# Kernel tuning notes

Measured on AMD Instinct MI355X. Metric: run time of the kernel, lower is better.

The kernel has to match this reference:

```python
import jax, jax.numpy as jnp
import numpy as np
import math

B, S, H, NH = 2, 2048, 2048, 16
D = H // NH            # head dim = 128
FF = 4 * H
EPS = 1e-5


def layer_norm(x, w, b):
    mu = jnp.mean(x, axis=-1, keepdims=True)
    var = jnp.mean((x - mu) ** 2, axis=-1, keepdims=True)
    return (x - mu) * jax.lax.rsqrt(var + EPS) * w + b


def rotate_half(x):
    # split last dim into two halves (j=2 grouping), return (-x2, x1)
    x1, x2 = jnp.split(x, 2, axis=-1)
    return jnp.concatenate((-x2, x1), axis=-1)


def rope_freqs(seq_len, dim):
    inv_freq = 1.0 / (10000.0 ** (jnp.arange(0, dim, 2, dtype=jnp.float32) / dim))
    freqs = jnp.arange(seq_len, dtype=jnp.float32)[:, None] * inv_freq[None, :]
    return jnp.concatenate((freqs, freqs), axis=-1)  # [S, D]


def setup_inputs() -> dict:
    key = jax.random.key(0)
    ks = jax.random.split(key, 8)
    sc_h = 1.0 / math.sqrt(H)
    sc_ff = 1.0 / math.sqrt(FF)
    return {
        "hidden_states": jax.random.normal(ks[0], (B, S, H), jnp.float32),
        "attention_mask": jnp.zeros((1, 1, S, S), jnp.bool_),
        "ln1_w": jnp.ones((H,), jnp.float32),
        "ln1_b": jnp.zeros((H,), jnp.float32),
        "wqkv": jax.random.uniform(ks[1], (3 * H, H), jnp.float32, -sc_h, sc_h),
        "bqkv": jnp.zeros((3 * H,), jnp.float32),
        "wdense": jax.random.uniform(ks[2], (H, H), jnp.float32, -sc_h, sc_h),
        "bdense": jnp.zeros((H,), jnp.float32),
        "ln2_w": jnp.ones((H,), jnp.float32),
        "ln2_b": jnp.zeros((H,), jnp.float32),
        "w1": jax.random.uniform(ks[3], (FF, H), jnp.float32, -sc_h, sc_h),
        "b1": jnp.zeros((FF,), jnp.float32),
        "w2": jax.random.uniform(ks[4], (H, FF), jnp.float32, -sc_ff, sc_ff),
        "b2": jnp.zeros((H,), jnp.float32),
    }


def reference(hidden_states, attention_mask, ln1_w, ln1_b, wqkv, bqkv,
              wdense, bdense, ln2_w, ln2_b, w1, b1, w2, b2):
    residual = hidden_states
    x = layer_norm(hidden_states, ln1_w, ln1_b)

    qkv = jnp.einsum('bsh,oh->bso', x, wqkv) + bqkv           # [B,S,3H]
    qkv = qkv.reshape(B, S, NH, 3 * D).transpose(0, 2, 1, 3)  # [B,NH,S,3D]
    q, k, v = jnp.split(qkv, 3, axis=-1)                      # each [B,NH,S,D]

    pos = rope_freqs(S, D)                                    # [S,D]
    cos, sin = jnp.cos(pos), jnp.sin(pos)
    q = q * cos + rotate_half(q) * sin
    k = k * cos + rotate_half(k) * sin

    scale = 1.0 / math.sqrt(D)
    scores = jnp.einsum('bhqd,bhkd->bhqk', q, k) * scale      # [B,NH,S,S]
    causal = jnp.tril(jnp.ones((S, S), jnp.bool_))
    scores = jnp.where(causal, scores.astype(jnp.float32), -1e9)
    probs = jax.nn.softmax(scores, axis=-1).astype(v.dtype)

    ctx = jnp.einsum('bhqk,bhkd->bhqd', probs, v)             # [B,NH,S,D]
    ctx = ctx.transpose(0, 2, 1, 3).reshape(B, S, H)
    attn_out = jnp.einsum('bsh,oh->bso', ctx, wdense) + bdense

    hidden = residual + attn_out
    residual = hidden
    x = layer_norm(hidden, ln2_w, ln2_b)
    inter = jax.nn.gelu(jnp.einsum('bsh,fh->bsf', x, w1) + b1, approximate=False)
    out = jnp.einsum('bsf,hf->bsh', inter, w2) + b2
    hidden = residual + out
    return (hidden, attention_mask)
```

## Files before the change

### kernel.cpp

```cpp
#include <hip/hip_runtime.h>
#include <math.h>

typedef unsigned short u16;
typedef unsigned int u32;
typedef __attribute__((ext_vector_type(8))) __bf16 bf16x8;
typedef __attribute__((ext_vector_type(4))) float f32x4;
typedef __attribute__((ext_vector_type(8))) u16 u16x8;
typedef __attribute__((ext_vector_type(4))) u16 u16x4;

#define BB 2
#define SS 2048
#define HH 2048
#define NHH 16
#define DD 128
#define FFF 8192
#define MM (BB * SS)

__device__ __forceinline__ u16 f2bf(float f) {
  u32 u = __float_as_uint(f);
  u32 r = (u + 0x7FFFu + ((u >> 16) & 1u)) >> 16;
  return (u16)r;
}
__device__ __forceinline__ float b2f(u16 h) {
  return __uint_as_float(((u32)h) << 16);
}
__device__ __forceinline__ void gll16(const void* g, void* l) {
  __builtin_amdgcn_global_load_lds((const __attribute__((address_space(1))) void*)g,
                                   (__attribute__((address_space(3))) void*)l, 16, 0, 0);
}

struct CvtArgs {
  const float* src[4];
  u16* dst[4];
  int n[4];
};
__global__ __launch_bounds__(256) void cvt_all(CvtArgs a) {
  const int seg = blockIdx.y;
  const int i = (blockIdx.x * 256 + threadIdx.x) * 4;
  if (i + 3 < a.n[seg]) {
    f32x4 v = *(const f32x4*)(a.src[seg] + i);
    u16x4 o;
    o[0] = f2bf(v[0]); o[1] = f2bf(v[1]); o[2] = f2bf(v[2]); o[3] = f2bf(v[3]);
    *(u16x4*)(a.dst[seg] + i) = o;
  }
}

__global__ __launch_bounds__(256) void ln_bf16(const float* __restrict__ x,
                                               const float* __restrict__ w,
                                               const float* __restrict__ bsh,
                                               u16* __restrict__ out) {
  const int row = blockIdx.x, tid = threadIdx.x;
  const float* xr = x + (size_t)row * HH;
  f32x4 a = ((const f32x4*)xr)[tid * 2];
  f32x4 b = ((const f32x4*)xr)[tid * 2 + 1];
  float s = a[0] + a[1] + a[2] + a[3] + b[0] + b[1] + b[2] + b[3];
  float q = a[0]*a[0] + a[1]*a[1] + a[2]*a[2] + a[3]*a[3]
          + b[0]*b[0] + b[1]*b[1] + b[2]*b[2] + b[3]*b[3];
#pragma unroll
  for (int off = 32; off > 0; off >>= 1) {
    s += __shfl_down(s, off);
    q += __shfl_down(q, off);
  }
  __shared__ float red[8];
  const int wave = tid >> 6;
  if ((tid & 63) == 0) { red[wave] = s; red[4 + wave] = q; }
  __syncthreads();
  s = red[0] + red[1] + red[2] + red[3];
  q = red[4] + red[5] + red[6] + red[7];
  const float mean = s * (1.0f / HH);
  const float var = q * (1.0f / HH) - mean * mean;
  const float rstd = 1.0f / sqrtf(var + 1e-5f);
  f32x4 w0 = ((const f32x4*)w)[tid * 2];
  f32x4 w1 = ((const f32x4*)w)[tid * 2 + 1];
  f32x4 b0 = ((const f32x4*)bsh)[tid * 2];
  f32x4 b1 = ((const f32x4*)bsh)[tid * 2 + 1];
  u16x8 o;
#pragma unroll
  for (int i = 0; i < 4; ++i) o[i] = f2bf((a[i] - mean) * rstd * w0[i] + b0[i]);
#pragma unroll
  for (int i = 0; i < 4; ++i) o[4 + i] = f2bf((b[i] - mean) * rstd * w1[i] + b1[i]);
  *(u16x8*)(out + (size_t)row * HH + tid * 8) = o;
}

template <int MODE, int DB>
__global__ __launch_bounds__(256) void gemm_bt(const u16* __restrict__ A,
                                               const u16* __restrict__ Bw,
                                               const float* __restrict__ bias,
                                               const float* resid, void* Cout,
                                               int M, int N, int K) {
  __shared__ __align__(16) u16 As[DB ? 2 : 1][128 * 64];
  __shared__ __align__(16) u16 Bs[DB ? 2 : 1][128 * 64];
  const int tid = threadIdx.x;
  const int wave = tid >> 6, lane = tid & 63;
  const int l15 = lane & 15, quad = lane >> 4;
  const int bm = blockIdx.x, bn = blockIdx.y;
  const int wm = (wave >> 1) << 6, wn = (wave & 1) << 6;

  f32x4 acc[4][4] = {};

  const int srow = (wave << 5) + (lane >> 3);
  const int sg = (lane & 7) ^ (lane >> 3);
  const u16* aptr = A + (size_t)(bm * 128 + srow) * K + sg * 8;
  const u16* bptr = Bw + (size_t)(bn * 128 + srow) * K + sg * 8;

  auto stage = [&](int buf) {
#pragma unroll
    for (int i = 0; i < 4; ++i)
      gll16(aptr + (size_t)i * 8 * K, &As[buf][(wave * 4 + i) * 512]);
#pragma unroll
    for (int i = 0; i < 4; ++i)
      gll16(bptr + (size_t)i * 8 * K, &Bs[buf][(wave * 4 + i) * 512]);
    aptr += 64; bptr += 64;
  };

  auto compute = [&](int buf) {
#pragma unroll
    for (int tt = 0; tt < 2; ++tt) {
      bf16x8 af[4], bfv[4];
#pragma unroll
      for (int i = 0; i < 4; ++i) {
        const int m = wm + i * 16 + l15;
        const int n = wn + i * 16 + l15;
        const int gi = tt * 4 + quad;
        af[i] = *(const bf16x8*)&As[buf][m * 64 + ((gi ^ (m & 7)) << 3)];
        bfv[i] = *(const bf16x8*)&Bs[buf][n * 64 + ((gi ^ (n & 7)) << 3)];
      }
#pragma unroll
      for (int i = 0; i < 4; ++i)
#pragma unroll
        for (int j = 0; j < 4; ++j)
          acc[i][j] = __builtin_amdgcn_mfma_f32_16x16x32_bf16(af[i], bfv[j], acc[i][j], 0, 0, 0);
    }
  };

  const int nk = K >> 6;
  if constexpr (DB) {
    stage(0);
    for (int kt = 0; kt < nk; ++kt) {
      __syncthreads();
      if (kt + 1 < nk) stage((kt + 1) & 1);
      compute(kt & 1);
    }
  } else {
    for (int kt = 0; kt < nk; ++kt) {
      stage(0);
      __syncthreads();
      compute(0);
      __syncthreads();
    }
  }

#pragma unroll
  for (int i = 0; i < 4; ++i) {
    const int row0 = bm * 128 + wm + i * 16 + quad * 4;
#pragma unroll
    for (int j = 0; j < 4; ++j) {
      const int col = bn * 128 + wn + j * 16 + l15;
      const float bv = bias[col];
#pragma unroll
      for (int r = 0; r < 4; ++r) {
        const size_t idx = (size_t)(row0 + r) * N + col;
        float v = acc[i][j][r] + bv;
        if constexpr (MODE == 0) {
          ((u16*)Cout)[idx] = f2bf(v);
        } else if constexpr (MODE == 1) {
          ((float*)Cout)[idx] = v + resid[idx];
        } else {
          v = 0.5f * v * (1.0f + erff(v * 0.70710678118654752f));
          ((u16*)Cout)[idx] = f2bf(v);
        }
      }
    }
  }
}

#define PHASE256(QM, QN, STG, DW)                                                              \
  do {                                                                                         \
    bf16x8 af[4][2], bq[2][2];                                                                 \
    _Pragma("unroll") for (int im = 0; im < 4; ++im) {                                         \
      const int ar = wm * 128 + (QM) * 64 + im * 16 + l15;                                     \
      _Pragma("unroll") for (int tt = 0; tt < 2; ++tt)                                         \
          af[im][tt] = *(const bf16x8*)&as[ar * 64 + ((((tt << 2) + quad) ^ (ar & 7)) << 3)];  \
    }                                                                                          \
    _Pragma("unroll") for (int jn = 0; jn < 2; ++jn) {                                         \
      const int br = wn * 64 + (QN) * 32 + jn * 16 + l15;                                      \
      _Pragma("unroll") for (int tt = 0; tt < 2; ++tt)                                         \
          bq[jn][tt] = *(const bf16x8*)&bs[br * 64 + ((((tt << 2) + quad) ^ (br & 7)) << 3)];  \
    }                                                                                          \
    STG;                                                                                       \
    __builtin_amdgcn_s_barrier();                                                              \
    asm volatile("s_waitcnt lgkmcnt(0)" ::: "memory");                                         \
    __builtin_amdgcn_sched_barrier(0);                                                         \
    __builtin_amdgcn_s_setprio(1);                                                             \
    _Pragma("unroll") for (int tt = 0; tt < 2; ++tt)                                           \
        _Pragma("unroll") for (int im = 0; im < 4; ++im)                                       \
            _Pragma("unroll") for (int jn = 0; jn < 2; ++jn)                                   \
                acc[(QM) * 4 + im][(QN) * 2 + jn] = __builtin_amdgcn_mfma_f32_16x16x32_bf16(   \
                    af[im][tt], bq[jn][tt], acc[(QM) * 4 + im][(QN) * 2 + jn], 0, 0, 0);       \
    __builtin_amdgcn_s_setprio(0);                                                             \
    if (DW) {                                                                                  \
      asm volatile("s_waitcnt vmcnt(4)" ::: "memory");                                         \
      __builtin_amdgcn_sched_barrier(0);                                                       \
    }                                                                                          \
    __builtin_amdgcn_s_barrier();                                                              \
  } while (0)

template <int MODE>
__global__ __launch_bounds__(512, 2) void gemm256(const u16* __restrict__ A,
                                                  const u16* __restrict__ Bw,
                                                  const float* __restrict__ bias,
                                                  void* Cout, int M, int N, int K) {
  __shared__ __align__(16) u16 As[2][256 * 64];
  __shared__ __align__(16) u16 Bs[2][256 * 64];
  const int tid = threadIdx.x;
  const int wave = tid >> 6, lane = tid & 63;
  const int l15 = lane & 15, quad = lane >> 4;
  const int wm = wave >> 2, wn = wave & 3;
  const int bm = blockIdx.x, bn = blockIdx.y;

  f32x4 acc[8][4] = {};

  const size_t loff = (size_t)(lane >> 3) * K + (size_t)(((lane & 7) ^ (lane >> 3)) << 3);
  const u16* Abase = A + (size_t)(bm * 256) * K + loff;
  const u16* Bbase = Bw + (size_t)(bn * 256) * K + loff;

  auto stageA = [&](int buf, int kt, int h) {
#pragma unroll
    for (int i = 0; i < 2; ++i) {
      const int c = wave * 2 + i;
      const int rb = ((c & 8) << 4) | (h * 64 + (c & 7) * 8);
      gll16(Abase + (size_t)rb * K + kt * 64, &As[buf][rb * 64]);
    }
  };
  auto stageB = [&](int buf, int kt, int h) {
#pragma unroll
    for (int i = 0; i < 2; ++i) {
      const int c = wave * 2 + i;
      const int rb = (c >> 2) * 64 + h * 32 + (c & 3) * 8;
      gll16(Bbase + (size_t)rb * K + kt * 64, &Bs[buf][rb * 64]);
    }
  };

  const int nk = K >> 6;
  stageA(0, 0, 0); stageB(0, 0, 0); stageA(0, 0, 1); stageB(0, 0, 1);
  asm volatile("s_waitcnt vmcnt(4)" ::: "memory");
  __builtin_amdgcn_sched_barrier(0);
  __builtin_amdgcn_s_barrier();

  for (int kt = 0; kt < nk; ++kt) {
    const int cb = kt & 1, ob = cb ^ 1;
    const u16* as = As[cb];
    const u16* bs = Bs[cb];
    const bool pf = (kt + 1 < nk);
    PHASE256(0, 0, { if (pf) stageA(ob, kt + 1, 0); }, 1);
    PHASE256(1, 0, { if (pf) stageB(ob, kt + 1, 0); }, 1);
    PHASE256(1, 1, { if (pf) stageA(ob, kt + 1, 1); }, 0);
    PHASE256(0, 1, { if (pf) stageB(ob, kt + 1, 1); }, 1);
  }

#pragma unroll
  for (int i = 0; i < 8; ++i) {
    const int row0 = bm * 256 + wm * 128 + (i >> 2) * 64 + (i & 3) * 16 + quad * 4;
#pragma unroll
    for (int j = 0; j < 4; ++j) {
      const int col = bn * 256 + wn * 64 + (j >> 1) * 32 + (j & 1) * 16 + l15;
      const float bv = bias[col];
#pragma unroll
      for (int r = 0; r < 4; ++r) {
        const size_t idx = (size_t)(row0 + r) * N + col;
        float v = acc[i][j][r] + bv;
        if constexpr (MODE == 0) {
          ((u16*)Cout)[idx] = f2bf(v);
        } else {
          v = 0.5f * v * (1.0f + erff(v * 0.70710678118654752f));
          ((u16*)Cout)[idx] = f2bf(v);
        }
      }
    }
  }
}

__global__ __launch_bounds__(256) void rope_kernel(const u16* __restrict__ qkv,
                                                   u16* __restrict__ Qr,
                                                   u16* __restrict__ Kr) {
  const int tid = threadIdx.x;
  const int d = tid & 63;
  const int s = blockIdx.x * 4 + (tid >> 6);
  const int h = blockIdx.y, b = blockIdx.z;
  const u16* row = qkv + ((size_t)(b * SS + s)) * (3 * HH) + h * (3 * DD);
  const float q1 = b2f(row[d]),        q2 = b2f(row[d + 64]);
  const float k1 = b2f(row[DD + d]),   k2 = b2f(row[DD + d + 64]);
  const float inv = expf((float)d * -0.14391156830963714f);
  const float ang = (float)s * inv;
  const float cs = cosf(ang), sn = sinf(ang);
  const size_t o = ((size_t)(b * NHH + h) * SS + s) * DD;
  Qr[o + d]      = f2bf(q1 * cs - q2 * sn);
  Qr[o + d + 64] = f2bf(q2 * cs + q1 * sn);
  Kr[o + d]      = f2bf(k1 * cs - k2 * sn);
  Kr[o + d + 64] = f2bf(k2 * cs + k1 * sn);
}

__device__ __forceinline__ int vslot(int s, int chunk) {
  return chunk ^ (s & 7) ^ ((s >> 3) & 7);
}
__global__ __launch_bounds__(256) void vtrans(const u16* __restrict__ qkv,
                                              u16* __restrict__ Vt) {
  __shared__ __align__(16) u16 Vs[64 * 128];
  const int tid = threadIdx.x;
  const int s0 = blockIdx.x * 64;
  const int bh = blockIdx.y;
  const int b = bh >> 4, h = bh & 15;
  const u16* src = qkv + (size_t)(b * SS + s0) * (3 * HH) + h * (3 * DD) + 2 * DD;
#pragma unroll
  for (int rr = 0; rr < 4; ++rr) {
    const int task = tid + rr * 256;
    const int sr = task >> 4, c = task & 15;
    u16x8 v = *(const u16x8*)(src + (size_t)sr * (3 * HH) + c * 8);
    const int sl = (vslot(sr, c & 7) | (c & 8));
    *(u16x8*)&Vs[sr * 128 + sl * 8] = v;
  }
  __syncthreads();
#pragma unroll
  for (int rr = 0; rr < 4; ++rr) {
    const int task = tid + rr * 256;
    const int dr = task >> 3, c = task & 7;
    u16x8 o;
#pragma unroll
    for (int e = 0; e < 8; ++e) {
      const int s = c * 8 + e;
      const int sl = (vslot(s, dr >> 3 & 7) | ((dr >> 3) & 8));
      o[e] = Vs[s * 128 + sl * 8 + (dr & 7)];
    }
    *(u16x8*)(Vt + (size_t)(bh * DD + dr) * SS + s0 + c * 8) = o;
  }
}

__device__ __forceinline__ void softmax_pv(f32x4 s4[4], bool diag, int qrl0,
                                           float m_run[4], float l_run[4],
                                           f32x4 oacc[8], const u16* vtb,
                                           u16* psw, int quad, int l15) {
  const float SCL = 0.12751742904630190f;
  float pv[4][4];
  float mx[4] = {-3e38f, -3e38f, -3e38f, -3e38f};
#pragma unroll
  for (int jt = 0; jt < 4; ++jt)
#pragma unroll
    for (int r = 0; r < 4; ++r) {
      float sv = s4[jt][r] * SCL;
      if (diag && (jt * 16 + l15) > (qrl0 + r)) sv = -3e38f;
      pv[jt][r] = sv;
      mx[r] = fmaxf(mx[r], sv);
    }
#pragma unroll
  for (int r = 0; r < 4; ++r) {
    mx[r] = fmaxf(mx[r], __shfl_xor(mx[r], 1));
    mx[r] = fmaxf(mx[r], __shfl_xor(mx[r], 2));
    mx[r] = fmaxf(mx[r], __shfl_xor(mx[r], 4));
    mx[r] = fmaxf(mx[r], __shfl_xor(mx[r], 8));
  }
  float al[4];
#pragma unroll
  for (int r = 0; r < 4; ++r) {
    const float mnew = fmaxf(m_run[r], mx[r]);
    al[r] = exp2f(m_run[r] - mnew);
    m_run[r] = mnew;
  }
  float rs[4] = {0.f, 0.f, 0.f, 0.f};
#pragma unroll
  for (int jt = 0; jt < 4; ++jt)
#pragma unroll
    for (int r = 0; r < 4; ++r) {
      const float pp = exp2f(pv[jt][r] - m_run[r]);
      pv[jt][r] = pp;
      rs[r] += pp;
    }
#pragma unroll
  for (int r = 0; r < 4; ++r) {
    rs[r] += __shfl_xor(rs[r], 1);
    rs[r] += __shfl_xor(rs[r], 2);
    rs[r] += __shfl_xor(rs[r], 4);
    rs[r] += __shfl_xor(rs[r], 8);
    l_run[r] = l_run[r] * al[r] + rs[r];
  }
#pragma unroll
  for (int jn = 0; jn < 8; ++jn)
#pragma unroll
    for (int r = 0; r < 4; ++r) oacc[jn][r] *= al[r];
#pragma unroll
  for (int jt = 0; jt < 4; ++jt)
#pragma unroll
    for (int r = 0; r < 4; ++r) {
      const int qr = quad * 4 + r, key = jt * 16 + l15;
      psw[qr * 64 + (((key >> 3) ^ (qr & 7)) << 3) + (key & 7)] = f2bf(pv[jt][r]);
    }
  __threadfence_block();
#pragma unroll
  for (int t = 0; t < 2; ++t) {
    const int gg = t * 4 + quad;
    bf16x8 pf = *(const bf16x8*)&psw[l15 * 64 + ((gg ^ (l15 & 7)) << 3)];
#pragma unroll
    for (int jn = 0; jn < 8; ++jn) {
      const int nd = jn * 16 + l15;
      bf16x8 vf = *(const bf16x8*)&vtb[nd * 64 + ((gg ^ (nd & 7)) << 3)];
      oacc[jn] = __builtin_amdgcn_mfma_f32_16x16x32_bf16(pf, vf, oacc[jn], 0, 0, 0);
    }
  }
}

__global__ __launch_bounds__(256, 2) void attn_kernel(const u16* __restrict__ Q,
                                                      const u16* __restrict__ Kg,
                                                      const u16* __restrict__ Vtg,
                                                      u16* __restrict__ ctx) {
  __shared__ __align__(16) u16 Ks[2][64 * 128];
  __shared__ __align__(16) u16 Vt[2][128 * 64];
  __shared__ __align__(16) u16 Ps[4][16 * 64];
  const int tid = threadIdx.x;
  const int wave = tid >> 6, lane = tid & 63;
  const int l15 = lane & 15, quad = lane >> 4;
  const int p = blockIdx.x, h = blockIdx.y, b = blockIdx.z;
  const int qlo = p, qhi = 31 - p;
  const size_t bh = (size_t)(b * NHH + h);
  const u16* Qp = Q + bh * ((size_t)SS * DD);
  const u16* Kp = Kg + bh * ((size_t)SS * DD);
  const u16* Vp = Vtg + bh * ((size_t)DD * SS);

  bf16x8 qfl[4], qfh[4];
  {
    const u16* ql = Qp + (size_t)(qlo * 64 + wave * 16 + l15) * DD + quad * 8;
    const u16* qh = Qp + (size_t)(qhi * 64 + wave * 16 + l15) * DD + quad * 8;
#pragma unroll
    for (int t = 0; t < 4; ++t) {
      qfl[t] = *(const bf16x8*)(ql + t * 32);
      qfh[t] = *(const bf16x8*)(qh + t * 32);
    }
  }

  f32x4 oal[8] = {}, oah[8] = {};
  float ml[4] = {-3e38f, -3e38f, -3e38f, -3e38f};
  float mh[4] = {-3e38f, -3e38f, -3e38f, -3e38f};
  float ll[4] = {0.f, 0.f, 0.f, 0.f}, lh[4] = {0.f, 0.f, 0.f, 0.f};

  auto stage = [&](int kt, int bufi) {
    const int k0 = kt * 64;
#pragma unroll
    for (int i = 0; i < 4; ++i) {
      const int g = wave * 4 + i;
      const int r = g * 4 + quad;
      const int c = l15 ^ (r & 15);
      gll16(Kp + (size_t)(k0 + r) * DD + c * 8, &Ks[bufi][g * 512]);
    }
#pragma unroll
    for (int i = 0; i < 4; ++i) {
      const int g = wave * 4 + i;
      const int d = g * 8 + (lane >> 3);
      const int c = (lane & 7) ^ (d & 7);
      gll16(Vp + (size_t)d * SS + k0 + c * 8, &Vt[bufi][g * 512]);
    }
  };

  stage(0, 0);
  const int qrl0 = wave * 16 + quad * 4;
  for (int kt = 0; kt <= qhi; ++kt) {
    __syncthreads();
    const u16* ksb = Ks[kt & 1];
    const u16* vtb = Vt[kt & 1];
    if (kt < qhi) stage(kt + 1, (kt + 1) & 1);
    const bool lo = (kt <= qlo);

    f32x4 sh4[4] = {}, sl4[4] = {};
#pragma unroll
    for (int t = 0; t < 4; ++t)
#pragma unroll
      for (int jt = 0; jt < 4; ++jt) {
        const int key = jt * 16 + l15;
        bf16x8 kf = *(const bf16x8*)&ksb[key * 128 + (((t * 4 + quad) ^ (key & 15)) << 3)];
        sh4[jt] = __builtin_amdgcn_mfma_f32_16x16x32_bf16(qfh[t], kf, sh4[jt], 0, 0, 0);
        if (lo) sl4[jt] = __builtin_amdgcn_mfma_f32_16x16x32_bf16(qfl[t], kf, sl4[jt], 0, 0, 0);
      }

    softmax_pv(sh4, kt == qhi, qrl0, mh, lh, oah, vtb, Ps[wave], quad, l15);
    if (lo) softmax_pv(sl4, kt == qlo, qrl0, ml, ll, oal, vtb, Ps[wave], quad, l15);
  }

  float invh[4], invl[4];
#pragma unroll
  for (int r = 0; r < 4; ++r) { invh[r] = 1.0f / lh[r]; invl[r] = 1.0f / ll[r]; }
#pragma unroll
  for (int jn = 0; jn < 8; ++jn)
#pragma unroll
    for (int r = 0; r < 4; ++r) {
      const int col = h * DD + jn * 16 + l15;
      const int rh = qhi * 64 + qrl0 + r;
      const int rl = qlo * 64 + qrl0 + r;
      ctx[(size_t)(b * SS + rh) * HH + col] = f2bf(oah[jn][r] * invh[r]);
      ctx[(size_t)(b * SS + rl) * HH + col] = f2bf(oal[jn][r] * invl[r]);
    }
}

extern "C" void kernel_launch(void* const* d_in, const int* in_sizes, int n_in,
                              void* d_out, int out_size, void* d_ws, size_t ws_size,
                              hipStream_t stream) {
  (void)in_sizes; (void)n_in; (void)ws_size;
  const float* hidden = (const float*)d_in[0];
  const float* ln1w = (const float*)d_in[2];
  const float* ln1b = (const float*)d_in[3];
  const float* wqkv = (const float*)d_in[4];
  const float* bqkv = (const float*)d_in[5];
  const float* wdense = (const float*)d_in[6];
  const float* bdense = (const float*)d_in[7];
  const float* ln2w = (const float*)d_in[8];
  const float* ln2b = (const float*)d_in[9];
  const float* w1 = (const float*)d_in[10];
  const float* b1 = (const float*)d_in[11];
  const float* w2 = (const float*)d_in[12];
  const float* b2 = (const float*)d_in[13];

  char* ws = (char*)d_ws;
  size_t off = 0;
  auto alloc = [&](size_t elems) {
    u16* p = (u16*)(ws + off);
    off += ((elems * 2 + 255) & ~(size_t)255);
    return p;
  };
  u16* wqkvbf = alloc((size_t)3 * HH * HH);
  u16* wdbf   = alloc((size_t)HH * HH);
  u16* w1bf   = alloc((size_t)FFF * HH);
  u16* w2bf   = alloc((size_t)HH * FFF);
  u16* xbf    = alloc((size_t)MM * HH);
  u16* ctx    = alloc((size_t)MM * HH);
  u16* big    = alloc((size_t)MM * 3 * HH + 3 * (size_t)BB * NHH * SS * DD);
  u16* qkvbuf = big;
  u16* Qr = big + (size_t)MM * 3 * HH;
  u16* Kr = Qr + (size_t)BB * NHH * SS * DD;
  u16* Vtg = Kr + (size_t)BB * NHH * SS * DD;
  u16* inter = big;

  CvtArgs ca;
  ca.src[0] = wqkv;   ca.dst[0] = wqkvbf; ca.n[0] = 3 * HH * HH;
  ca.src[1] = wdense; ca.dst[1] = wdbf;   ca.n[1] = HH * HH;
  ca.src[2] = w1;     ca.dst[2] = w1bf;   ca.n[2] = FFF * HH;
  ca.src[3] = w2;     ca.dst[3] = w2bf;   ca.n[3] = HH * FFF;
  cvt_all<<<dim3((FFF * HH) / 1024, 4), 256, 0, stream>>>(ca);

  ln_bf16<<<MM, 256, 0, stream>>>(hidden, ln1w, ln1b, xbf);
  gemm256<0><<<dim3(MM / 256, (3 * HH) / 256), 512, 0, stream>>>(
      xbf, wqkvbf, bqkv, qkvbuf, MM, 3 * HH, HH);
  rope_kernel<<<dim3(SS / 4, NHH, BB), 256, 0, stream>>>(qkvbuf, Qr, Kr);
  vtrans<<<dim3(SS / 64, BB * NHH), 256, 0, stream>>>(qkvbuf, Vtg);
  attn_kernel<<<dim3(16, NHH, BB), 256, 0, stream>>>(Qr, Kr, Vtg, ctx);
  gemm_bt<1, 1><<<dim3(MM / 128, HH / 128), 256, 0, stream>>>(
      ctx, wdbf, bdense, hidden, d_out, MM, HH, HH);
  ln_bf16<<<MM, 256, 0, stream>>>((const float*)d_out, ln2w, ln2b, xbf);
  gemm256<2><<<dim3(MM / 256, FFF / 256), 512, 0, stream>>>(
      xbf, w1bf, b1, inter, MM, FFF, HH);
  gemm_bt<1, 1><<<dim3(MM / 128, HH / 128), 256, 0, stream>>>(
      inter, w2bf, b2, (const float*)d_out, d_out, MM, HH, FFF);

  const size_t hid_elems = (size_t)MM * HH;
  if ((size_t)out_size > hid_elems)
    hipMemsetAsync((char*)d_out + hid_elems * 4, 0,
                   ((size_t)out_size - hid_elems) * 4, stream);
}
```

Before: 1.056 ms.

## Reuse LDS operand fragments across GEMM sub-phases and cut per-phase barriers

```diff
diff --git a/kernel.cpp b/kernel.cpp
--- a/kernel.cpp
+++ b/kernel.cpp
@@ -174,37 +174,6 @@
   }
 }
 
-#define PHASE256(QM, QN, STG, DW)                                                              \
-  do {                                                                                         \
-    bf16x8 af[4][2], bq[2][2];                                                                 \
-    _Pragma("unroll") for (int im = 0; im < 4; ++im) {                                         \
-      const int ar = wm * 128 + (QM) * 64 + im * 16 + l15;                                     \
-      _Pragma("unroll") for (int tt = 0; tt < 2; ++tt)                                         \
-          af[im][tt] = *(const bf16x8*)&as[ar * 64 + ((((tt << 2) + quad) ^ (ar & 7)) << 3)];  \
-    }                                                                                          \
-    _Pragma("unroll") for (int jn = 0; jn < 2; ++jn) {                                         \
-      const int br = wn * 64 + (QN) * 32 + jn * 16 + l15;                                      \
-      _Pragma("unroll") for (int tt = 0; tt < 2; ++tt)                                         \
-          bq[jn][tt] = *(const bf16x8*)&bs[br * 64 + ((((tt << 2) + quad) ^ (br & 7)) << 3)];  \
-    }                                                                                          \
-    STG;                                                                                       \
-    __builtin_amdgcn_s_barrier();                                                              \
-    asm volatile("s_waitcnt lgkmcnt(0)" ::: "memory");                                         \
-    __builtin_amdgcn_sched_barrier(0);                                                         \
-    __builtin_amdgcn_s_setprio(1);                                                             \
-    _Pragma("unroll") for (int tt = 0; tt < 2; ++tt)                                           \
-        _Pragma("unroll") for (int im = 0; im < 4; ++im)                                       \
-            _Pragma("unroll") for (int jn = 0; jn < 2; ++jn)                                   \
-                acc[(QM) * 4 + im][(QN) * 2 + jn] = __builtin_amdgcn_mfma_f32_16x16x32_bf16(   \
-                    af[im][tt], bq[jn][tt], acc[(QM) * 4 + im][(QN) * 2 + jn], 0, 0, 0);       \
-    __builtin_amdgcn_s_setprio(0);                                                             \
-    if (DW) {                                                                                  \
-      asm volatile("s_waitcnt vmcnt(4)" ::: "memory");                                         \
-      __builtin_amdgcn_sched_barrier(0);                                                       \
-    }                                                                                          \
-    __builtin_amdgcn_s_barrier();                                                              \
-  } while (0)
-
 template <int MODE>
 __global__ __launch_bounds__(512, 2) void gemm256(const u16* __restrict__ A,
                                                   const u16* __restrict__ Bw,
@@ -241,6 +210,37 @@
     }
   };
 
+  auto ldA = [&](const u16* as_, int qm, bf16x8 (&dst)[4][2]) {
+#pragma unroll
+    for (int im = 0; im < 4; ++im) {
+      const int ar = wm * 128 + qm * 64 + im * 16 + l15;
+#pragma unroll
+      for (int tt = 0; tt < 2; ++tt)
+        dst[im][tt] = *(const bf16x8*)&as_[ar * 64 + ((((tt << 2) + quad) ^ (ar & 7)) << 3)];
+    }
+  };
+  auto ldB = [&](const u16* bs_, int qn, bf16x8 (&dst)[2][2]) {
+#pragma unroll
+    for (int jn = 0; jn < 2; ++jn) {
+      const int br = wn * 64 + qn * 32 + jn * 16 + l15;
+#pragma unroll
+      for (int tt = 0; tt < 2; ++tt)
+        dst[jn][tt] = *(const bf16x8*)&bs_[br * 64 + ((((tt << 2) + quad) ^ (br & 7)) << 3)];
+    }
+  };
+  auto mm = [&](bf16x8 (&a)[4][2], bf16x8 (&b)[2][2], int i0, int j0) {
+    __builtin_amdgcn_s_setprio(1);
+#pragma unroll
+    for (int tt = 0; tt < 2; ++tt)
+#pragma unroll
+      for (int im = 0; im < 4; ++im)
+#pragma unroll
+        for (int jn = 0; jn < 2; ++jn)
+          acc[i0 + im][j0 + jn] = __builtin_amdgcn_mfma_f32_16x16x32_bf16(
+              a[im][tt], b[jn][tt], acc[i0 + im][j0 + jn], 0, 0, 0);
+    __builtin_amdgcn_s_setprio(0);
+  };
+
   const int nk = K >> 6;
   stageA(0, 0, 0); stageB(0, 0, 0); stageA(0, 0, 1); stageB(0, 0, 1);
   asm volatile("s_waitcnt vmcnt(4)" ::: "memory");
@@ -249,21 +249,46 @@
 
   for (int kt = 0; kt < nk; ++kt) {
     const int cb = kt & 1, ob = cb ^ 1;
-    const u16* as = As[cb];
-    const u16* bs = Bs[cb];
+    const u16* as_ = As[cb];
+    const u16* bs_ = Bs[cb];
     const bool pf = (kt + 1 < nk);
-    PHASE256(0, 0, { if (pf) stageA(ob, kt + 1, 0); }, 1);
-    PHASE256(1, 0, { if (pf) stageB(ob, kt + 1, 0); }, 1);
-    PHASE256(1, 1, { if (pf) stageA(ob, kt + 1, 1); }, 0);
-    PHASE256(0, 1, { if (pf) stageB(ob, kt + 1, 1); }, 1);
+    bf16x8 a0[4][2], a1[4][2], b0[2][2], b1[2][2];
+
+    ldA(as_, 0, a0);
+    ldB(bs_, 0, b0);
+    if (pf) stageA(ob, kt + 1, 0);
+    mm(a0, b0, 0, 0);
+    if (pf) asm volatile("s_waitcnt vmcnt(4)" ::: "memory");
+    else    asm volatile("s_waitcnt vmcnt(2)" ::: "memory");
+    __builtin_amdgcn_sched_barrier(0);
+    __builtin_amdgcn_s_barrier();
+
+    ldA(as_, 1, a1);
+    if (pf) stageB(ob, kt + 1, 0);
+    mm(a1, b0, 4, 0);
+    if (pf) asm volatile("s_waitcnt vmcnt(4)" ::: "memory");
+    else    asm volatile("s_waitcnt vmcnt(0)" ::: "memory");
+    __builtin_amdgcn_sched_barrier(0);
+    __builtin_amdgcn_s_barrier();
+
+    ldB(bs_, 1, b1);
+    if (pf) stageA(ob, kt + 1, 1);
+    mm(a1, b1, 4, 2);
+    if (pf) stageB(ob, kt + 1, 1);
+    mm(a0, b1, 0, 2);
+    if (pf) {
+      asm volatile("s_waitcnt vmcnt(4)" ::: "memory");
+      __builtin_amdgcn_sched_barrier(0);
+    }
+    __builtin_amdgcn_s_barrier();
   }
 
 #pragma unroll
   for (int i = 0; i < 8; ++i) {
-    const int row0 = bm * 256 + wm * 128 + (i >> 2) * 64 + (i & 3) * 16 + quad * 4;
+    const int row0 = bm * 256 + wm * 128 + i * 16 + quad * 4;
 #pragma unroll
     for (int j = 0; j < 4; ++j) {
-      const int col = bn * 256 + wn * 64 + (j >> 1) * 32 + (j & 1) * 16 + l15;
+      const int col = bn * 256 + wn * 64 + j * 16 + l15;
       const float bv = bias[col];
 #pragma unroll
       for (int r = 0; r < 4; ++r) {
```

After: 915.3 us. -13.3%, faster.
